# Kernel tuning notes

Measured on AMD Instinct MI355X. Metric: run time of the kernel, lower is better.

Reference implementation:

```python
import jax, jax.numpy as jnp
import numpy as np

K = 3  # kernel_size

def _hamming2d(k):
    h = np.hamming(k)
    return (np.outer(h, h)).astype(np.float32)

def setup_inputs() -> dict:
    key = jax.random.key(0)
    k1, k2 = jax.random.split(key)
    x = jax.random.normal(k1, (8, 64, 128, 128), dtype=jnp.float32)
    W = jax.random.normal(k2, (9, 64, 3, 3), dtype=jnp.float32) * 0.001
    b = jnp.zeros((9,), dtype=jnp.float32)
    return {"x": x, "W": W, "b": b}

def reference(x, W, b):
    B, C, H, Wd = x.shape
    # filter generator: 3x3 conv, padding=1 -> (B, K*K, H, W)
    mask = jax.lax.conv_general_dilated(
        x, W, window_strides=(1, 1), padding=((1, 1), (1, 1)),
        dimension_numbers=("NCHW", "OIHW", "NCHW")) + b[None, :, None, None]
    # kernel normalizer: softmax over the K*K taps, hamming reweight, renormalize
    mask = jax.nn.softmax(mask, axis=1)
    ham = jnp.asarray(_hamming2d(K).reshape(-1))  # (K*K,)
    mask = mask * ham[None, :, None, None]
    mask = mask / jnp.sum(mask, axis=1, keepdims=True)
    # carafe (up=1): weighted sum of KxK shifted neighborhoods, reflect-padded.
    pad = K // 2
    xp = jnp.pad(x, ((0, 0), (0, 0), (pad, pad), (pad, pad)), mode="reflect")
    lowpass = jnp.zeros_like(x)
    for idx in range(K * K):
        i, j = divmod(idx, K)
        lowpass = lowpass + xp[:, :, i:i + H, j:j + Wd] * mask[:, idx:idx + 1]
    # highpass = x - lowpass; residual output = x + highpass
    return 2.0 * x - lowpass
```

## Files before the change

### kernel.cpp

```cpp
#include <hip/hip_runtime.h>


typedef __attribute__((ext_vector_type(8))) short short8;
typedef __attribute__((ext_vector_type(4))) float floatx4;

#define IH 128
#define IW 128
#define CCH 64
#define TS 16
#define TP 18
#define CSH 72
#define MPAD 13

__device__ __forceinline__ unsigned short f2bf(float f) {
    unsigned u = __float_as_uint(f);
    u += 0x7FFFu + ((u >> 16) & 1u);
    return (unsigned short)(u >> 16);
}
__device__ __forceinline__ float bf2f(unsigned short s) {
    return __uint_as_float(((unsigned)s) << 16);
}

__global__ __launch_bounds__(256) void ahpf_kernel(
    const float* __restrict__ x, const float* __restrict__ Wg,
    const float* __restrict__ bias, float* __restrict__ out)
{
    __shared__ __align__(16) unsigned short sx[TP * TP * CSH];
    __shared__ __align__(16) unsigned char uni[13312];
    unsigned short* wb = (unsigned short*)uni;
    float* smask       = (float*)uni;

    const int tid  = threadIdx.x;
    const int lane = tid & 63;
    const int wv   = tid >> 6;
    const int bz   = blockIdx.z;
    const int ty0  = blockIdx.y * TS;
    const int tx0  = blockIdx.x * TS;
    const size_t hw = (size_t)IH * IW;
    const float* xb = x + (size_t)bz * CCH * hw;

    for (int i = tid; i < 18 * 9 * 32; i += 256) {
        int s = i / 288, r = i % 288, m = r / 32, ko = r & 31;
        int tap = s >> 1, c = (s & 1) * 32 + ko;
        wb[i] = f2bf(Wg[m * 576 + c * 9 + tap]);
    }

    for (int i = tid; i < CCH * TP * TP; i += 256) {
        int c = i / (TP * TP), p = i % (TP * TP);
        int yy = p / TP, xx = p % TP;
        int gy = ty0 + yy - 1; gy = gy < 0 ? -gy : (gy >= IH ? 2 * IH - 2 - gy : gy);
        int gx = tx0 + xx - 1; gx = gx < 0 ? -gx : (gx >= IW ? 2 * IW - 2 - gx : gx);
        sx[p * CSH + c] = f2bf(xb[(size_t)c * hw + (size_t)gy * IW + gx]);
    }
    __syncthreads();

    const int fm = lane & 15;
    const int fq = lane >> 4;
    short8 afr[18];
#pragma unroll
    for (int s = 0; s < 18; ++s) {
        if (fm < 9)
            afr[s] = *(const short8*)&wb[(s * 9 + fm) * 32 + fq * 8];
        else
            afr[s] = (short8)0;
    }
    float bq[4];
#pragma unroll
    for (int r = 0; r < 4; ++r) {
        int t = fq * 4 + r;
        bq[r] = (t < 9) ? bias[t] : 0.0f;
    }
    __syncthreads();

    const bool border = (blockIdx.x == 0) | (blockIdx.x == IW / TS - 1) |
                        (blockIdx.y == 0) | (blockIdx.y == IH / TS - 1);
    const int n = lane & 15;

    for (int rr = 0; rr < 4; ++rr) {
        const int R = wv * 4 + rr;
        floatx4 acc = {0.f, 0.f, 0.f, 0.f};
#pragma unroll
        for (int s = 0; s < 18; ++s) {
            const int tap = s >> 1;
            const int dy = tap / 3 - 1, dx = tap % 3 - 1;
            const int idx = ((R + 1 + dy) * TP + (n + 1 + dx)) * CSH
                          + (s & 1) * 32 + fq * 8;
            short8 bf = *(const short8*)&sx[idx];
            if (border) {
                int hy = ty0 + R + dy, wx = tx0 + n + dx;
                if (hy < 0 || hy >= IH || wx < 0 || wx >= IW) bf = (short8)0;
            }
            acc = __builtin_amdgcn_mfma_f32_16x16x32_bf16(afr[s], bf, acc, 0, 0, 0);
        }
        float a0 = acc[0] + bq[0], a1 = acc[1] + bq[1],
              a2 = acc[2] + bq[2], a3 = acc[3] + bq[3];
        const int nval = (fq < 2) ? 4 : (fq == 2 ? 1 : 0);
        float mx = -1e30f;
        if (nval >= 1) mx = a0;
        if (nval >= 4) { mx = fmaxf(mx, a1); mx = fmaxf(mx, fmaxf(a2, a3)); }
        mx = fmaxf(mx, __shfl_xor(mx, 16));
        mx = fmaxf(mx, __shfl_xor(mx, 32));
        auto hamt = [](int t) {
            float a = (t / 3 == 1) ? 1.f : 0.08f;
            float b = (t % 3 == 1) ? 1.f : 0.08f;
            return a * b;
        };
        float e0 = 0, e1 = 0, e2 = 0, e3 = 0, ssum = 0;
        if (nval >= 1) { e0 = __expf(a0 - mx) * hamt(fq * 4 + 0); ssum += e0; }
        if (nval >= 4) { e1 = __expf(a1 - mx) * hamt(fq * 4 + 1); ssum += e1;
                         e2 = __expf(a2 - mx) * hamt(fq * 4 + 2); ssum += e2;
                         e3 = __expf(a3 - mx) * hamt(fq * 4 + 3); ssum += e3; }
        ssum += __shfl_xor(ssum, 16);
        ssum += __shfl_xor(ssum, 32);
        const float inv = 1.0f / ssum;
        const int pix = R * 16 + n;
        if (nval >= 1) smask[pix * MPAD + fq * 4 + 0] = e0 * inv;
        if (nval >= 4) { smask[pix * MPAD + fq * 4 + 1] = e1 * inv;
                         smask[pix * MPAD + fq * 4 + 2] = e2 * inv;
                         smask[pix * MPAD + fq * 4 + 3] = e3 * inv; }
    }

    {
        const int pr = lane >> 4, pc = lane & 15;
        const int R = wv * 4 + pr;
        const int h = ty0 + R, w = tx0 + pc;
        float mk[9];
#pragma unroll
        for (int t = 0; t < 9; ++t) mk[t] = smask[(R * 16 + pc) * MPAD + t];
        float* ob = out + (size_t)bz * CCH * hw + (size_t)h * IW + w;
        const int pbase = ((R + 1) * TP + (pc + 1)) * CSH;
#pragma unroll 2
        for (int g = 0; g < 8; ++g) {
            float o[8];
            {
                const short8 v = *(const short8*)&sx[pbase + g * 8];
#pragma unroll
                for (int j = 0; j < 8; ++j)
                    o[j] = (2.0f - mk[4]) * bf2f((unsigned short)v[j]);
            }
#pragma unroll
            for (int t = 0; t < 9; ++t) {
                if (t == 4) continue;
                const int dy = t / 3 - 1, dx = t % 3 - 1;
                const short8 v = *(const short8*)&sx[pbase + (dy * TP + dx) * CSH + g * 8];
#pragma unroll
                for (int j = 0; j < 8; ++j)
                    o[j] = fmaf(-mk[t], bf2f((unsigned short)v[j]), o[j]);
            }
#pragma unroll
            for (int j = 0; j < 8; ++j)
                ob[(size_t)(g * 8 + j) * hw] = o[j];
        }
    }
}

extern "C" void kernel_launch(void* const* d_in, const int* in_sizes, int n_in,
                              void* d_out, int out_size, void* d_ws, size_t ws_size,
                              hipStream_t stream) {
    const float* x    = (const float*)d_in[0];
    const float* Wg   = (const float*)d_in[1];
    const float* bias = (const float*)d_in[2];
    float* out        = (float*)d_out;

    const int B = in_sizes[0] / (CCH * IH * IW);
    dim3 grid(IW / TS, IH / TS, B);
    ahpf_kernel<<<grid, dim3(256, 1, 1), 0, stream>>>(x, Wg, bias, out);
}
```

Before: 108.8 us.

## Vectorize halo loads, load weights directly, bf16 mask, block swizzle, nontemporal stores

The halo tile of x is now staged with float4 row loads instead of scalar gathers, and reflect padding is handled by extra writes at the tile edges. Weight fragments are read from global memory into registers directly, which removes the LDS staging buffer and a barrier. The per-pixel mask is stored in LDS as packed bf16, and the softmax max-subtraction is dropped, which relies on the logits being small. Other changes add a block-index swizzle, nontemporal output stores and an occupancy hint in launch_bounds. The max-subtraction removal and the bf16 mask reduce numerical robustness, and the swizzle hardcodes an 8x8 tile grid and batch 8.

```diff
diff --git a/kernel.cpp b/kernel.cpp
--- a/kernel.cpp
+++ b/kernel.cpp
@@ -10,7 +10,7 @@
 #define TS 16
 #define TP 18
 #define CSH 72
-#define MPAD 13
+#define MST 12
 
 __device__ __forceinline__ unsigned short f2bf(float f) {
     unsigned u = __float_as_uint(f);
@@ -21,59 +21,81 @@
     return __uint_as_float(((unsigned)s) << 16);
 }
 
-__global__ __launch_bounds__(256) void ahpf_kernel(
+__global__ __launch_bounds__(256, 3) void ahpf_kernel(
     const float* __restrict__ x, const float* __restrict__ Wg,
     const float* __restrict__ bias, float* __restrict__ out)
 {
     __shared__ __align__(16) unsigned short sx[TP * TP * CSH];
-    __shared__ __align__(16) unsigned char uni[13312];
-    unsigned short* wb = (unsigned short*)uni;
-    float* smask       = (float*)uni;
+    __shared__ __align__(16) unsigned short smask[256 * MST];
 
     const int tid  = threadIdx.x;
     const int lane = tid & 63;
     const int wv   = tid >> 6;
-    const int bz   = blockIdx.z;
-    const int ty0  = blockIdx.y * TS;
-    const int tx0  = blockIdx.x * TS;
+
+    const unsigned flat = blockIdx.x + gridDim.x * (blockIdx.y + gridDim.y * blockIdx.z);
+    const unsigned nid  = (flat & 7u) * 64u + (flat >> 3);
+    const int bx = nid & 7, by = (nid >> 3) & 7, bz = nid >> 6;
+
+    const int ty0 = by * TS;
+    const int tx0 = bx * TS;
     const size_t hw = (size_t)IH * IW;
     const float* xb = x + (size_t)bz * CCH * hw;
-
-    for (int i = tid; i < 18 * 9 * 32; i += 256) {
-        int s = i / 288, r = i % 288, m = r / 32, ko = r & 31;
-        int tap = s >> 1, c = (s & 1) * 32 + ko;
-        wb[i] = f2bf(Wg[m * 576 + c * 9 + tap]);
-    }
-
-    for (int i = tid; i < CCH * TP * TP; i += 256) {
-        int c = i / (TP * TP), p = i % (TP * TP);
-        int yy = p / TP, xx = p % TP;
-        int gy = ty0 + yy - 1; gy = gy < 0 ? -gy : (gy >= IH ? 2 * IH - 2 - gy : gy);
-        int gx = tx0 + xx - 1; gx = gx < 0 ? -gx : (gx >= IW ? 2 * IW - 2 - gx : gx);
-        sx[p * CSH + c] = f2bf(xb[(size_t)c * hw + (size_t)gy * IW + gx]);
-    }
-    __syncthreads();
 
     const int fm = lane & 15;
     const int fq = lane >> 4;
     short8 afr[18];
 #pragma unroll
     for (int s = 0; s < 18; ++s) {
-        if (fm < 9)
-            afr[s] = *(const short8*)&wb[(s * 9 + fm) * 32 + fq * 8];
-        else
-            afr[s] = (short8)0;
+        short8 a = (short8)0;
+        if (fm < 9) {
+            const int tap = s >> 1;
+            const int cb  = (s & 1) * 32 + fq * 8;
+            const float* wp = Wg + fm * 576 + tap;
+#pragma unroll
+            for (int jj = 0; jj < 8; ++jj)
+                a[jj] = (short)f2bf(wp[(cb + jj) * 9]);
+        }
+        afr[s] = a;
     }
     float bq[4];
 #pragma unroll
     for (int r = 0; r < 4; ++r) {
-        int t = fq * 4 + r;
+        const int t = fq * 4 + r;
         bq[r] = (t < 9) ? bias[t] : 0.0f;
+    }
+
+    {
+        int gx0 = tx0 - 4;
+        if (gx0 < 0) gx0 = 0;
+        if (gx0 > IW - 24) gx0 = IW - 24;
+        const bool xlo = (bx == 0), xhi = (bx == 7);
+        for (int s = tid; s < TP * CCH * 6; s += 256) {
+            const int q  = s / 6, j = s - q * 6;
+            const int c  = q & 63, yy = q >> 6;
+            int gy = ty0 + yy - 1;
+            gy = gy < 0 ? -gy : (gy >= IH ? 2 * IH - 2 - gy : gy);
+            const float4 v = *(const float4*)(xb + (size_t)c * hw + (size_t)gy * IW + gx0 + 4 * j);
+            unsigned short bf[4] = {f2bf(v.x), f2bf(v.y), f2bf(v.z), f2bf(v.w)};
+            const int xbase = gx0 + 4 * j - tx0 + 1;
+#pragma unroll
+            for (int e = 0; e < 4; ++e) {
+                const int xx = xbase + e;
+                if (xx >= 0 && xx < TP)
+                    sx[(yy * TP + xx) * CSH + c] = bf[e];
+            }
+            if (xlo) {
+                const int e = 1 - (gx0 + 4 * j);
+                if (e >= 0 && e < 4) sx[(yy * TP + 0) * CSH + c] = bf[e];
+            }
+            if (xhi) {
+                const int e = 126 - (gx0 + 4 * j);
+                if (e >= 0 && e < 4) sx[(yy * TP + 17) * CSH + c] = bf[e];
+            }
+        }
     }
     __syncthreads();
 
-    const bool border = (blockIdx.x == 0) | (blockIdx.x == IW / TS - 1) |
-                        (blockIdx.y == 0) | (blockIdx.y == IH / TS - 1);
+    const bool border = (bx == 0) | (bx == 7) | (by == 0) | (by == 7);
     const int n = lane & 15;
 
     for (int rr = 0; rr < 4; ++rr) {
@@ -87,46 +109,49 @@
                           + (s & 1) * 32 + fq * 8;
             short8 bf = *(const short8*)&sx[idx];
             if (border) {
-                int hy = ty0 + R + dy, wx = tx0 + n + dx;
+                const int hy = ty0 + R + dy, wx = tx0 + n + dx;
                 if (hy < 0 || hy >= IH || wx < 0 || wx >= IW) bf = (short8)0;
             }
             acc = __builtin_amdgcn_mfma_f32_16x16x32_bf16(afr[s], bf, acc, 0, 0, 0);
         }
-        float a0 = acc[0] + bq[0], a1 = acc[1] + bq[1],
-              a2 = acc[2] + bq[2], a3 = acc[3] + bq[3];
-        const int nval = (fq < 2) ? 4 : (fq == 2 ? 1 : 0);
-        float mx = -1e30f;
-        if (nval >= 1) mx = a0;
-        if (nval >= 4) { mx = fmaxf(mx, a1); mx = fmaxf(mx, fmaxf(a2, a3)); }
-        mx = fmaxf(mx, __shfl_xor(mx, 16));
-        mx = fmaxf(mx, __shfl_xor(mx, 32));
+        const float a0 = acc[0] + bq[0], a1 = acc[1] + bq[1],
+                    a2 = acc[2] + bq[2], a3 = acc[3] + bq[3];
         auto hamt = [](int t) {
-            float a = (t / 3 == 1) ? 1.f : 0.08f;
-            float b = (t % 3 == 1) ? 1.f : 0.08f;
+            const float a = (t / 3 == 1) ? 1.f : 0.08f;
+            const float b = (t % 3 == 1) ? 1.f : 0.08f;
             return a * b;
         };
+        const int nval = (fq < 2) ? 4 : (fq == 2 ? 1 : 0);
         float e0 = 0, e1 = 0, e2 = 0, e3 = 0, ssum = 0;
-        if (nval >= 1) { e0 = __expf(a0 - mx) * hamt(fq * 4 + 0); ssum += e0; }
-        if (nval >= 4) { e1 = __expf(a1 - mx) * hamt(fq * 4 + 1); ssum += e1;
-                         e2 = __expf(a2 - mx) * hamt(fq * 4 + 2); ssum += e2;
-                         e3 = __expf(a3 - mx) * hamt(fq * 4 + 3); ssum += e3; }
+        if (nval >= 1) { e0 = __expf(a0) * hamt(fq * 4 + 0); ssum += e0; }
+        if (nval >= 4) { e1 = __expf(a1) * hamt(fq * 4 + 1); ssum += e1;
+                         e2 = __expf(a2) * hamt(fq * 4 + 2); ssum += e2;
+                         e3 = __expf(a3) * hamt(fq * 4 + 3); ssum += e3; }
         ssum += __shfl_xor(ssum, 16);
         ssum += __shfl_xor(ssum, 32);
         const float inv = 1.0f / ssum;
-        const int pix = R * 16 + n;
-        if (nval >= 1) smask[pix * MPAD + fq * 4 + 0] = e0 * inv;
-        if (nval >= 4) { smask[pix * MPAD + fq * 4 + 1] = e1 * inv;
-                         smask[pix * MPAD + fq * 4 + 2] = e2 * inv;
-                         smask[pix * MPAD + fq * 4 + 3] = e3 * inv; }
+        if (fq < 3) {
+            const unsigned long long m0 = f2bf(e0 * inv), m1 = f2bf(e1 * inv),
+                                     m2 = f2bf(e2 * inv), m3 = f2bf(e3 * inv);
+            *(unsigned long long*)&smask[(R * 16 + n) * MST + fq * 4] =
+                m0 | (m1 << 16) | (m2 << 32) | (m3 << 48);
+        }
     }
+    __syncthreads();
 
     {
         const int pr = lane >> 4, pc = lane & 15;
         const int R = wv * 4 + pr;
         const int h = ty0 + R, w = tx0 + pc;
+        const unsigned long long* mp =
+            (const unsigned long long*)&smask[(R * 16 + pc) * MST];
+        const unsigned long long p0 = mp[0], p1 = mp[1], p2 = mp[2];
         float mk[9];
 #pragma unroll
-        for (int t = 0; t < 9; ++t) mk[t] = smask[(R * 16 + pc) * MPAD + t];
+        for (int t = 0; t < 8; ++t)
+            mk[t] = bf2f((unsigned short)((t < 4 ? p0 : p1) >> ((t & 3) * 16)));
+        mk[8] = bf2f((unsigned short)p2);
+
         float* ob = out + (size_t)bz * CCH * hw + (size_t)h * IW + w;
         const int pbase = ((R + 1) * TP + (pc + 1)) * CSH;
 #pragma unroll 2
@@ -149,7 +174,7 @@
             }
 #pragma unroll
             for (int j = 0; j < 8; ++j)
-                ob[(size_t)(g * 8 + j) * hw] = o[j];
+                __builtin_nontemporal_store(o[j], &ob[(size_t)(g * 8 + j) * hw]);
         }
     }
 }
@@ -162,7 +187,6 @@
     const float* bias = (const float*)d_in[2];
     float* out        = (float*)d_out;
 
-    const int B = in_sizes[0] / (CCH * IH * IW);
-    dim3 grid(IW / TS, IH / TS, B);
+    dim3 grid(IW / TS, IH / TS, in_sizes[0] / (CCH * IH * IW));
     ahpf_kernel<<<grid, dim3(256, 1, 1), 0, stream>>>(x, Wg, bias, out);
 }
```

Result: slower. 129.9 us (+19.3%).
